# Kernel optimization log

Measured on AMD Instinct MI355X. Metric: run time of the kernel, lower is better.

The kernel has to match this reference:

```python
import jax, jax.numpy as jnp
import numpy as np

B, S = 2, 1024          # 2 sequences of 1024 tokens (prefill)
HID = 2880
HQ, HKV, D = 64, 8, 64  # query heads, kv heads, head_dim
W = 128                 # sliding window size
THETA = 150000.0
SCALE = D ** -0.5
Q_SIZE, KV_SIZE = HQ * D, HKV * D


def _rope_neox(pos, x):
    # pos: [T] int, x: [T, H, D] -> neox-style full-dim rotary
    half = D // 2
    inv_freq = 1.0 / (THETA ** (jnp.arange(half, dtype=jnp.float32) * 2.0 / D))
    ang = pos.astype(jnp.float32)[:, None] * inv_freq          # [T, D/2]
    cos = jnp.cos(ang)[:, None, :]                             # [T, 1, D/2]
    sin = jnp.sin(ang)[:, None, :]
    x1, x2 = x[..., :half], x[..., half:]
    return jnp.concatenate([x1 * cos - x2 * sin, x1 * sin + x2 * cos], axis=-1)


def setup_inputs() -> dict:
    key = jax.random.key(0)
    ks = jax.random.split(key, 10)
    s = 0.02
    hidden_states = jax.random.normal(ks[0], (B * S, HID), dtype=jnp.float32)
    positions = jnp.tile(jnp.arange(S, dtype=jnp.int32), B)    # per-sequence positions
    Wq = jax.random.normal(ks[1], (HID, Q_SIZE), dtype=jnp.float32) * s
    bq = jax.random.normal(ks[2], (Q_SIZE,), dtype=jnp.float32) * s
    Wk = jax.random.normal(ks[3], (HID, KV_SIZE), dtype=jnp.float32) * s
    bk = jax.random.normal(ks[4], (KV_SIZE,), dtype=jnp.float32) * s
    Wv = jax.random.normal(ks[5], (HID, KV_SIZE), dtype=jnp.float32) * s
    bv = jax.random.normal(ks[6], (KV_SIZE,), dtype=jnp.float32) * s
    Wo = jax.random.normal(ks[7], (Q_SIZE, HID), dtype=jnp.float32) * s
    bo = jax.random.normal(ks[8], (HID,), dtype=jnp.float32) * s
    return {"hidden_states": hidden_states, "positions": positions,
            "Wq": Wq, "bq": bq, "Wk": Wk, "bk": bk,
            "Wv": Wv, "bv": bv, "Wo": Wo, "bo": bo}


def reference(hidden_states, positions, Wq, bq, Wk, bk, Wv, bv, Wo, bo):
    T = hidden_states.shape[0]
    q = (hidden_states @ Wq + bq).reshape(T, HQ, D)
    k = (hidden_states @ Wk + bk).reshape(T, HKV, D)
    v = (hidden_states @ Wv + bv).reshape(T, HKV, D)
    q = _rope_neox(positions, q)
    k = _rope_neox(positions, k)

    # sliding-window causal attention (banded, window = last W keys + self)
    G = HQ // HKV  # GQA group size
    q5 = q.reshape(B, S, HKV, G, D)
    k4 = k.reshape(B, S, HKV, D)
    v4 = v.reshape(B, S, HKV, D)
    offs = jnp.arange(W + 1)
    idx = jnp.arange(S)[:, None] - W + offs[None, :]           # [S, W+1] key index j
    valid = idx >= 0                                           # causal+window band
    idx_c = jnp.clip(idx, 0, S - 1)
    kw = k4[:, idx_c]                                          # [B, S, W+1, HKV, D]
    vw = v4[:, idx_c]
    scores = jnp.einsum('bikgd,biwkd->bikgw', q5, kw) * SCALE  # [B,S,HKV,G,W+1]
    scores = jnp.where(valid[None, :, None, None, :], scores, jnp.float32(-1e30))
    p = jax.nn.softmax(scores, axis=-1)
    o = jnp.einsum('bikgw,biwkd->bikgd', p, vw).reshape(T, Q_SIZE)
    return o @ Wo + bo


if __name__ == '__main__':
    out = reference(**setup_inputs())
    print(out.shape, out.dtype)
```

## Files before the change

### kernel.cpp

```cpp
#include <hip/hip_runtime.h>

#define T_TOK 2048
#define S_LEN 1024
#define HIDN  2880
#define NHQ   64
#define NHKV  8
#define DH    64
#define QSZ   4096
#define KVSZ  512
#define WIN   128
#define NQKV  5120
#define NOPAD 2944

typedef __attribute__((ext_vector_type(4))) float f32x4;
typedef __attribute__((ext_vector_type(8))) short bf16x8;
typedef __attribute__((ext_vector_type(4))) short s16x4;

__device__ __forceinline__ unsigned short f2bf(float f) {
  unsigned u = __float_as_uint(f);
  u += 0x7fffu + ((u >> 16) & 1u);
  return (unsigned short)(u >> 16);
}
__device__ __forceinline__ float bf2f(unsigned short s) {
  return __uint_as_float(((unsigned)s) << 16);
}
__device__ __forceinline__ void ld_g2l16(const void* g, void* l) {
  __builtin_amdgcn_global_load_lds(
      (const __attribute__((address_space(1))) unsigned int*)g,
      (__attribute__((address_space(3))) unsigned int*)l, 16, 0, 0);
}

__global__ __launch_bounds__(256) void convert_hidden(
    const float* __restrict__ in, unsigned short* __restrict__ out)
{
  const size_t off = ((size_t)blockIdx.x * 256 + threadIdx.x) * 8;
  const f32x4 a = *(const f32x4*)(in + off);
  const f32x4 b = *(const f32x4*)(in + off + 4);
  bf16x8 p;
  p[0] = (short)f2bf(a[0]); p[1] = (short)f2bf(a[1]);
  p[2] = (short)f2bf(a[2]); p[3] = (short)f2bf(a[3]);
  p[4] = (short)f2bf(b[0]); p[5] = (short)f2bf(b[1]);
  p[6] = (short)f2bf(b[2]); p[7] = (short)f2bf(b[3]);
  *(bf16x8*)(out + off) = p;
}

__global__ __launch_bounds__(256) void transpose_w(
    const float* __restrict__ W, unsigned short* __restrict__ WT,
    int K, int N)
{
  __shared__ float tile[32][65];
  const int tid = threadIdx.x;
  const int nb = blockIdx.x * 64;
  const int kb = blockIdx.y * 32;
  {
    const int n2 = (tid & 31) * 2;
    const int k0 = tid >> 5;
    #pragma unroll
    for (int r = 0; r < 4; ++r) {
      const int k = k0 + r * 8;
      const int gn = nb + n2;
      const size_t base = (size_t)(kb + k) * N;
      tile[k][n2]     = (gn     < N) ? W[base + gn]     : 0.f;
      tile[k][n2 + 1] = (gn + 1 < N) ? W[base + gn + 1] : 0.f;
    }
  }
  __syncthreads();
  {
    const int k4 = (tid & 7) * 4;
    const int n0 = tid >> 3;
    #pragma unroll
    for (int r = 0; r < 2; ++r) {
      const int n = n0 + r * 32;
      s16x4 p;
      p[0] = (short)f2bf(tile[k4][n]);     p[1] = (short)f2bf(tile[k4 + 1][n]);
      p[2] = (short)f2bf(tile[k4 + 2][n]); p[3] = (short)f2bf(tile[k4 + 3][n]);
      *(s16x4*)(WT + (size_t)(nb + n) * K + kb + k4) = p;
    }
  }
}

__device__ __forceinline__ void gemm_core(
    const unsigned short* __restrict__ A, const unsigned short* __restrict__ BT,
    int K, int m0, int n0, unsigned short* As, unsigned short* Bs,
    f32x4 acc[4][4])
{
  const int tid  = threadIdx.x;
  const int lane = tid & 63;
  const int wid  = tid >> 6;
  const int wm = (wid >> 1) * 64;
  const int wn = (wid & 1) * 64;
  const int fr = lane & 15;
  const int fq = lane >> 4;

  const int rsub = tid >> 3;
  const int cg   = (tid & 7) ^ (rsub & 7);
  const unsigned short* Ap = A  + (size_t)(m0 + rsub) * K + cg * 8;
  const unsigned short* Bp = BT + (size_t)(n0 + rsub) * K + cg * 8;
  const size_t rstep = (size_t)32 * K;

  for (int k0 = 0; k0 < K; k0 += 64) {
    #pragma unroll
    for (int i = 0; i < 4; ++i) {
      ld_g2l16(Ap + i * rstep + k0, As + ((size_t)i * 256 + tid) * 8);
      ld_g2l16(Bp + i * rstep + k0, Bs + ((size_t)i * 256 + tid) * 8);
    }
    __syncthreads();
    #pragma unroll
    for (int ks = 0; ks < 2; ++ks) {
      const int kc = ks * 4 + fq;
      bf16x8 af[4], bfr[4];
      #pragma unroll
      for (int mt = 0; mt < 4; ++mt) {
        const int R = wm + mt * 16 + fr;
        af[mt] = *(const bf16x8*)(As + R * 64 + ((kc ^ (R & 7)) << 3));
      }
      #pragma unroll
      for (int nt = 0; nt < 4; ++nt) {
        const int R = wn + nt * 16 + fr;
        bfr[nt] = *(const bf16x8*)(Bs + R * 64 + ((kc ^ (R & 7)) << 3));
      }
      #pragma unroll
      for (int mt = 0; mt < 4; ++mt)
        #pragma unroll
        for (int nt = 0; nt < 4; ++nt)
          acc[mt][nt] = __builtin_amdgcn_mfma_f32_16x16x32_bf16(
              af[mt], bfr[nt], acc[mt][nt], 0, 0, 0);
    }
    __syncthreads();
  }
}

__device__ __forceinline__ void rope_epilogue(
    f32x4 acc[4][4], const float* __restrict__ bias,
    const int* __restrict__ pos, unsigned short* __restrict__ outp,
    int outStride, int colbase, int rowbase, int lane)
{
  const int fr = lane & 15;
  const int r4 = (lane >> 4) * 4;
  const float invf0 = exp2f((float)fr        * (-17.19460283f / 32.0f));
  const float invf1 = exp2f((float)(fr + 16) * (-17.19460283f / 32.0f));
  #pragma unroll
  for (int mt = 0; mt < 4; ++mt) {
    #pragma unroll
    for (int i = 0; i < 4; ++i) {
      const int m = rowbase + mt * 16 + r4 + i;
      const float p = (float)pos[m];
      #pragma unroll
      for (int ntp = 0; ntp < 2; ++ntp) {
        float sv, cv;
        __sincosf(p * (ntp ? invf1 : invf0), &sv, &cv);
        const int c1 = colbase + ntp * 16 + fr;
        const float x1 = acc[mt][ntp][i]     + bias[c1];
        const float x2 = acc[mt][ntp + 2][i] + bias[c1 + 32];
        outp[(size_t)m * outStride + c1]      = f2bf(x1 * cv - x2 * sv);
        outp[(size_t)m * outStride + c1 + 32] = f2bf(x1 * sv + x2 * cv);
      }
    }
  }
}

__global__ __launch_bounds__(256) void gemm_qkv(
    const unsigned short* __restrict__ A, const unsigned short* __restrict__ BT,
    const float* __restrict__ bq, const float* __restrict__ bk,
    const float* __restrict__ bv, const int* __restrict__ pos,
    unsigned short* __restrict__ qb, unsigned short* __restrict__ kb,
    unsigned short* __restrict__ vT)
{
  __shared__ unsigned short As[128 * 64];
  __shared__ unsigned short Bs[128 * 64];
  const int m0 = blockIdx.y * 128;
  const int n0 = blockIdx.x * 128;
  f32x4 acc[4][4];
  #pragma unroll
  for (int i = 0; i < 4; ++i)
    #pragma unroll
    for (int j = 0; j < 4; ++j) acc[i][j] = (f32x4){0.f, 0.f, 0.f, 0.f};
  gemm_core(A, BT, HIDN, m0, n0, As, Bs, acc);

  const int lane = threadIdx.x & 63;
  const int wid  = threadIdx.x >> 6;
  const int wm = (wid >> 1) * 64;
  const int wn = (wid & 1) * 64;
  const int fr = lane & 15;
  const int r4 = (lane >> 4) * 4;

  if (n0 < QSZ) {
    rope_epilogue(acc, bq, pos, qb, QSZ, n0 + wn, m0 + wm, lane);
  } else if (n0 < QSZ + KVSZ) {
    rope_epilogue(acc, bk, pos, kb, KVSZ, n0 - QSZ + wn, m0 + wm, lane);
  } else {
    #pragma unroll
    for (int nt = 0; nt < 4; ++nt) {
      const int vrow = n0 - (QSZ + KVSZ) + wn + nt * 16 + fr;
      const float bvv = bv[vrow];
      #pragma unroll
      for (int mt = 0; mt < 4; ++mt) {
        const int mb = m0 + wm + mt * 16 + r4;
        s16x4 p;
        p[0] = (short)f2bf(acc[mt][nt][0] + bvv);
        p[1] = (short)f2bf(acc[mt][nt][1] + bvv);
        p[2] = (short)f2bf(acc[mt][nt][2] + bvv);
        p[3] = (short)f2bf(acc[mt][nt][3] + bvv);
        *(s16x4*)(vT + (size_t)vrow * T_TOK + mb) = p;
      }
    }
  }
}

__global__ __launch_bounds__(256) void gemm_o(
    const unsigned short* __restrict__ A, const unsigned short* __restrict__ BT,
    const float* __restrict__ bias, float* __restrict__ C)
{
  __shared__ unsigned short As[128 * 64];
  __shared__ unsigned short Bs[128 * 64];
  const int m0 = blockIdx.y * 128;
  const int n0 = blockIdx.x * 128;
  f32x4 acc[4][4];
  #pragma unroll
  for (int i = 0; i < 4; ++i)
    #pragma unroll
    for (int j = 0; j < 4; ++j) acc[i][j] = (f32x4){0.f, 0.f, 0.f, 0.f};
  gemm_core(A, BT, QSZ, m0, n0, As, Bs, acc);

  const int lane = threadIdx.x & 63;
  const int wid  = threadIdx.x >> 6;
  const int wm = (wid >> 1) * 64;
  const int wn = (wid & 1) * 64;
  const int fr = lane & 15;
  const int r4 = (lane >> 4) * 4;
  #pragma unroll
  for (int nt = 0; nt < 4; ++nt) {
    const int n = n0 + wn + nt * 16 + fr;
    if (n >= HIDN) continue;
    const float bvv = bias[n];
    #pragma unroll
    for (int mt = 0; mt < 4; ++mt) {
      const int mb = m0 + wm + mt * 16 + r4;
      #pragma unroll
      for (int i = 0; i < 4; ++i)
        C[(size_t)(mb + i) * HIDN + n] = acc[mt][nt][i] + bvv;
    }
  }
}

__global__ __launch_bounds__(256) void attn_kernel(
    const unsigned short* __restrict__ q, const unsigned short* __restrict__ k,
    const unsigned short* __restrict__ vT, unsigned short* __restrict__ o)
{
  __shared__ unsigned short lds[26624];
  unsigned short* Ks = lds;
  unsigned short* Qs = lds + 13824;
  unsigned short* Ps = lds + 13824;
  unsigned short* Vt = lds;

  const int tid  = threadIdx.x;
  const int lane = tid & 63;
  const int wid  = tid >> 6;
  const int sq0  = blockIdx.x * 64;
  const int h    = blockIdx.y;
  const int b    = blockIdx.z;
  const int kvh  = h >> 3;
  const int kp0  = sq0 - WIN;

  #pragma unroll
  for (int j = 0; j < 2; ++j) {
    const int c  = tid + j * 256;
    const int qr = c >> 3, dc = (c & 7) * 8;
    const bf16x8 vv = *(const bf16x8*)(
        q + (size_t)(b * S_LEN + sq0 + qr) * QSZ + h * DH + dc);
    *(bf16x8*)&Qs[qr * 72 + dc] = vv;
  }
  #pragma unroll
  for (int j = 0; j < 6; ++j) {
    const int c  = tid + j * 256;
    const int kr = c >> 3, dc = (c & 7) * 8;
    int tok = b * S_LEN + kp0 + kr;
    if (tok < 0) tok = 0;
    const bf16x8 vv = *(const bf16x8*)(k + (size_t)tok * KVSZ + kvh * DH + dc);
    *(bf16x8*)&Ks[kr * 72 + dc] = vv;
  }
  __syncthreads();

  const int fr = lane & 15;
  const int fk = (lane >> 4) * 8;
  const int qw = wid * 16;

  f32x4 S[12];
  #pragma unroll
  for (int i = 0; i < 12; ++i) S[i] = (f32x4){0.f, 0.f, 0.f, 0.f};
  #pragma unroll
  for (int ks = 0; ks < 2; ++ks) {
    const bf16x8 af = *(const bf16x8*)&Qs[(qw + fr) * 72 + ks * 32 + fk];
    #pragma unroll
    for (int nt = 0; nt < 12; ++nt) {
      const bf16x8 bfr = *(const bf16x8*)&Ks[(nt * 16 + fr) * 72 + ks * 32 + fk];
      S[nt] = __builtin_amdgcn_mfma_f32_16x16x32_bf16(af, bfr, S[nt], 0, 0, 0);
    }
  }

  const int qbase = sq0 + qw + ((lane >> 4) << 2);
  float lsum[4] = {0.f, 0.f, 0.f, 0.f};
  #pragma unroll
  for (int nt = 0; nt < 12; ++nt) {
    const int jpos = kp0 + nt * 16 + fr;
    #pragma unroll
    for (int i = 0; i < 4; ++i) {
      const int qa = qbase + i;
      const bool valid = (jpos >= 0) && (jpos <= qa) && (jpos >= qa - WIN);
      const float e = valid ? __expf(S[nt][i] * 0.125f) : 0.f;
      S[nt][i] = e;
      lsum[i] += e;
    }
  }
  #pragma unroll
  for (int off = 1; off < 16; off <<= 1)
    #pragma unroll
    for (int i = 0; i < 4; ++i)
      lsum[i] += __shfl_xor(lsum[i], off, 64);
  float inv[4];
  #pragma unroll
  for (int i = 0; i < 4; ++i) inv[i] = 1.0f / lsum[i];

  __syncthreads();

  #pragma unroll
  for (int nt = 0; nt < 12; ++nt)
    #pragma unroll
    for (int i = 0; i < 4; ++i)
      Ps[(qbase - sq0 + i) * 200 + nt * 16 + fr] = f2bf(S[nt][i]);

  if (kp0 >= 0) {
    #pragma unroll
    for (int j = 0; j < 6; ++j) {
      const int c  = tid + j * 256;
      const int dr = c / 24, kc = (c % 24) * 8;
      const bf16x8 vv = *(const bf16x8*)(
          vT + (size_t)(kvh * DH + dr) * T_TOK + b * S_LEN + kp0 + kc);
      *(bf16x8*)&Vt[dr * 200 + kc] = vv;
    }
  } else {
    #pragma unroll
    for (int j = 0; j < 6; ++j) {
      const int c  = tid + j * 256;
      const int dr = c / 24, kc = (c % 24) * 8;
      bf16x8 vv;
      #pragma unroll
      for (int u = 0; u < 8; ++u) {
        int col = b * S_LEN + kp0 + kc + u;
        if (col < 0) col = 0;
        vv[u] = (short)vT[(size_t)(kvh * DH + dr) * T_TOK + col];
      }
      *(bf16x8*)&Vt[dr * 200 + kc] = vv;
    }
  }
  __syncthreads();

  f32x4 O[4];
  #pragma unroll
  for (int i = 0; i < 4; ++i) O[i] = (f32x4){0.f, 0.f, 0.f, 0.f};
  #pragma unroll
  for (int ks = 0; ks < 6; ++ks) {
    const bf16x8 pa = *(const bf16x8*)&Ps[(qw + fr) * 200 + ks * 32 + fk];
    #pragma unroll
    for (int nt = 0; nt < 4; ++nt) {
      const bf16x8 vb = *(const bf16x8*)&Vt[(nt * 16 + fr) * 200 + ks * 32 + fk];
      O[nt] = __builtin_amdgcn_mfma_f32_16x16x32_bf16(pa, vb, O[nt], 0, 0, 0);
    }
  }
  #pragma unroll
  for (int nt = 0; nt < 4; ++nt)
    #pragma unroll
    for (int i = 0; i < 4; ++i)
      o[(size_t)(b * S_LEN + qbase + i) * QSZ + h * DH + nt * 16 + fr] =
          f2bf(O[nt][i] * inv[i]);
}

extern "C" void kernel_launch(void* const* d_in, const int* in_sizes, int n_in,
                              void* d_out, int out_size, void* d_ws, size_t ws_size,
                              hipStream_t stream) {
  const float* hidden    = (const float*)d_in[0];
  const int*   positions = (const int*)d_in[1];
  const float* Wq = (const float*)d_in[2];
  const float* bq = (const float*)d_in[3];
  const float* Wk = (const float*)d_in[4];
  const float* bk = (const float*)d_in[5];
  const float* Wv = (const float*)d_in[6];
  const float* bv = (const float*)d_in[7];
  const float* Wo = (const float*)d_in[8];
  const float* bo = (const float*)d_in[9];
  float* out = (float*)d_out;

  char* ws = (char*)d_ws;
  unsigned short* hbf   = (unsigned short*)(ws);
  unsigned short* WqkvT = (unsigned short*)(ws + 11796480);
  unsigned short* qb    = (unsigned short*)(ws + 41287680);
  unsigned short* kb    = (unsigned short*)(ws + 58064896);
  unsigned short* vTb   = (unsigned short*)(ws + 60162048);

  const dim3 blk(256);
  convert_hidden<<<dim3((T_TOK * HIDN) / 2048), blk, 0, stream>>>(hidden, hbf);
  transpose_w<<<dim3(QSZ / 64, HIDN / 32), blk, 0, stream>>>(
      Wq, WqkvT, HIDN, QSZ);
  transpose_w<<<dim3(KVSZ / 64, HIDN / 32), blk, 0, stream>>>(
      Wk, WqkvT + (size_t)QSZ * HIDN, HIDN, KVSZ);
  transpose_w<<<dim3(KVSZ / 64, HIDN / 32), blk, 0, stream>>>(
      Wv, WqkvT + (size_t)(QSZ + KVSZ) * HIDN, HIDN, KVSZ);

  gemm_qkv<<<dim3(NQKV / 128, T_TOK / 128), blk, 0, stream>>>(
      hbf, WqkvT, bq, bk, bv, positions, qb, kb, vTb);

  transpose_w<<<dim3(NOPAD / 64, QSZ / 32), blk, 0, stream>>>(
      Wo, WqkvT, QSZ, HIDN);

  attn_kernel<<<dim3(S_LEN / 64, NHQ, 2), blk, 0, stream>>>(qb, kb, vTb, qb);
  gemm_o<<<dim3(NOPAD / 128, T_TOK / 128), blk, 0, stream>>>(
      qb, WqkvT, bo, out);
}
```

Baseline: 400.2 us.

## Vectorize weight transpose, process two heads per attention block, shrink gemm_o tiles

transpose_w now reads eight floats per thread with vector loads, with a scalar fallback for the partial edge tile, and writes bf16x8 stores. The attention kernel processes two query heads per block so each K/V window load serves both heads, and Q fragments are loaded straight into registers instead of through LDS. gemm_o switches to 64x128 tiles with 128 threads, doubling the grid to improve CU occupancy for the small output GEMM. In exchange attention holds twice the score registers, and gemm_o loads each B tile for fewer output rows.

```diff
diff --git a/kernel.cpp b/kernel.cpp
--- a/kernel.cpp
+++ b/kernel.cpp
@@ -48,35 +48,29 @@
     const float* __restrict__ W, unsigned short* __restrict__ WT,
     int K, int N)
 {
-  __shared__ float tile[32][65];
+  __shared__ float tile[32][72];
   const int tid = threadIdx.x;
   const int nb = blockIdx.x * 64;
   const int kb = blockIdx.y * 32;
-  {
-    const int n2 = (tid & 31) * 2;
-    const int k0 = tid >> 5;
-    #pragma unroll
-    for (int r = 0; r < 4; ++r) {
-      const int k = k0 + r * 8;
-      const int gn = nb + n2;
-      const size_t base = (size_t)(kb + k) * N;
-      tile[k][n2]     = (gn     < N) ? W[base + gn]     : 0.f;
-      tile[k][n2 + 1] = (gn + 1 < N) ? W[base + gn + 1] : 0.f;
-    }
-  }
-  __syncthreads();
-  {
-    const int k4 = (tid & 7) * 4;
-    const int n0 = tid >> 3;
-    #pragma unroll
-    for (int r = 0; r < 2; ++r) {
-      const int n = n0 + r * 32;
-      s16x4 p;
-      p[0] = (short)f2bf(tile[k4][n]);     p[1] = (short)f2bf(tile[k4 + 1][n]);
-      p[2] = (short)f2bf(tile[k4 + 2][n]); p[3] = (short)f2bf(tile[k4 + 3][n]);
-      *(s16x4*)(WT + (size_t)(nb + n) * K + kb + k4) = p;
-    }
-  }
+  const int kk = tid >> 3;
+  const int n8 = (tid & 7) * 8;
+  if (nb + 64 <= N) {
+    const float* src = W + (size_t)(kb + kk) * N + nb + n8;
+    *(f32x4*)&tile[kk][n8]     = *(const f32x4*)(src);
+    *(f32x4*)&tile[kk][n8 + 4] = *(const f32x4*)(src + 4);
+  } else {
+    #pragma unroll
+    for (int u = 0; u < 8; ++u)
+      tile[kk][n8 + u] = (nb + n8 + u < N)
+          ? W[(size_t)(kb + kk) * N + nb + n8 + u] : 0.f;
+  }
+  __syncthreads();
+  const int n  = tid & 63;
+  const int k8 = (tid >> 6) * 8;
+  bf16x8 p;
+  #pragma unroll
+  for (int j = 0; j < 8; ++j) p[j] = (short)f2bf(tile[k8 + j][n]);
+  *(bf16x8*)(WT + (size_t)(nb + n) * K + kb + k8) = p;
 }
 
 __device__ __forceinline__ void gemm_core(
@@ -207,26 +201,65 @@
   }
 }
 
-__global__ __launch_bounds__(256) void gemm_o(
+__global__ __launch_bounds__(128) void gemm_o(
     const unsigned short* __restrict__ A, const unsigned short* __restrict__ BT,
     const float* __restrict__ bias, float* __restrict__ C)
 {
-  __shared__ unsigned short As[128 * 64];
+  __shared__ unsigned short As[64 * 64];
   __shared__ unsigned short Bs[128 * 64];
-  const int m0 = blockIdx.y * 128;
+  const int tid  = threadIdx.x;
+  const int lane = tid & 63;
+  const int wid  = tid >> 6;
+  const int m0 = blockIdx.y * 64;
   const int n0 = blockIdx.x * 128;
+  const int wn = wid * 64;
+  const int fr = lane & 15;
+  const int fq = lane >> 4;
+
   f32x4 acc[4][4];
   #pragma unroll
   for (int i = 0; i < 4; ++i)
     #pragma unroll
     for (int j = 0; j < 4; ++j) acc[i][j] = (f32x4){0.f, 0.f, 0.f, 0.f};
-  gemm_core(A, BT, QSZ, m0, n0, As, Bs, acc);
-
-  const int lane = threadIdx.x & 63;
-  const int wid  = threadIdx.x >> 6;
-  const int wm = (wid >> 1) * 64;
-  const int wn = (wid & 1) * 64;
-  const int fr = lane & 15;
+
+  const int rsub = tid >> 3;
+  const int cg   = (tid & 7) ^ (rsub & 7);
+  const unsigned short* Ap = A  + (size_t)(m0 + rsub) * QSZ + cg * 8;
+  const unsigned short* Bp = BT + (size_t)(n0 + rsub) * QSZ + cg * 8;
+  const size_t rstep = (size_t)16 * QSZ;
+
+  for (int k0 = 0; k0 < QSZ; k0 += 64) {
+    #pragma unroll
+    for (int i = 0; i < 4; ++i)
+      ld_g2l16(Ap + i * rstep + k0, As + ((size_t)i * 128 + tid) * 8);
+    #pragma unroll
+    for (int i = 0; i < 8; ++i)
+      ld_g2l16(Bp + i * rstep + k0, Bs + ((size_t)i * 128 + tid) * 8);
+    __syncthreads();
+    #pragma unroll
+    for (int ks = 0; ks < 2; ++ks) {
+      const int kc = ks * 4 + fq;
+      bf16x8 af[4], bfr[4];
+      #pragma unroll
+      for (int mt = 0; mt < 4; ++mt) {
+        const int R = mt * 16 + fr;
+        af[mt] = *(const bf16x8*)(As + R * 64 + ((kc ^ (R & 7)) << 3));
+      }
+      #pragma unroll
+      for (int nt = 0; nt < 4; ++nt) {
+        const int R = wn + nt * 16 + fr;
+        bfr[nt] = *(const bf16x8*)(Bs + R * 64 + ((kc ^ (R & 7)) << 3));
+      }
+      #pragma unroll
+      for (int mt = 0; mt < 4; ++mt)
+        #pragma unroll
+        for (int nt = 0; nt < 4; ++nt)
+          acc[mt][nt] = __builtin_amdgcn_mfma_f32_16x16x32_bf16(
+              af[mt], bfr[nt], acc[mt][nt], 0, 0, 0);
+    }
+    __syncthreads();
+  }
+
   const int r4 = (lane >> 4) * 4;
   #pragma unroll
   for (int nt = 0; nt < 4; ++nt) {
@@ -235,7 +268,7 @@
     const float bvv = bias[n];
     #pragma unroll
     for (int mt = 0; mt < 4; ++mt) {
-      const int mb = m0 + wm + mt * 16 + r4;
+      const int mb = m0 + mt * 16 + r4;
       #pragma unroll
       for (int i = 0; i < 4; ++i)
         C[(size_t)(mb + i) * HIDN + n] = acc[mt][nt][i] + bvv;
@@ -243,33 +276,39 @@
   }
 }
 
-__global__ __launch_bounds__(256) void attn_kernel(
+__global__ __launch_bounds__(256, 3) void attn_kernel(
     const unsigned short* __restrict__ q, const unsigned short* __restrict__ k,
     const unsigned short* __restrict__ vT, unsigned short* __restrict__ o)
 {
   __shared__ unsigned short lds[26624];
   unsigned short* Ks = lds;
-  unsigned short* Qs = lds + 13824;
+  unsigned short* Vt = lds;
   unsigned short* Ps = lds + 13824;
-  unsigned short* Vt = lds;
 
   const int tid  = threadIdx.x;
   const int lane = tid & 63;
   const int wid  = tid >> 6;
   const int sq0  = blockIdx.x * 64;
-  const int h    = blockIdx.y;
+  const int hp   = blockIdx.y;
   const int b    = blockIdx.z;
-  const int kvh  = h >> 3;
+  const int h0   = hp * 2;
+  const int kvh  = hp >> 2;
   const int kp0  = sq0 - WIN;
 
-  #pragma unroll
-  for (int j = 0; j < 2; ++j) {
-    const int c  = tid + j * 256;
-    const int qr = c >> 3, dc = (c & 7) * 8;
-    const bf16x8 vv = *(const bf16x8*)(
-        q + (size_t)(b * S_LEN + sq0 + qr) * QSZ + h * DH + dc);
-    *(bf16x8*)&Qs[qr * 72 + dc] = vv;
-  }
+  const int fr = lane & 15;
+  const int fk = (lane >> 4) * 8;
+  const int qw = wid * 16;
+
+  bf16x8 qf[2][2];
+  {
+    const size_t qrow = (size_t)(b * S_LEN + sq0 + qw + fr) * QSZ;
+    #pragma unroll
+    for (int hh = 0; hh < 2; ++hh)
+      #pragma unroll
+      for (int ks2 = 0; ks2 < 2; ++ks2)
+        qf[hh][ks2] = *(const bf16x8*)(q + qrow + (h0 + hh) * DH + ks2 * 32 + fk);
+  }
+
   #pragma unroll
   for (int j = 0; j < 6; ++j) {
     const int c  = tid + j * 256;
@@ -281,25 +320,25 @@
   }
   __syncthreads();
 
-  const int fr = lane & 15;
-  const int fk = (lane >> 4) * 8;
-  const int qw = wid * 16;
-
-  f32x4 S[12];
-  #pragma unroll
-  for (int i = 0; i < 12; ++i) S[i] = (f32x4){0.f, 0.f, 0.f, 0.f};
-  #pragma unroll
-  for (int ks = 0; ks < 2; ++ks) {
-    const bf16x8 af = *(const bf16x8*)&Qs[(qw + fr) * 72 + ks * 32 + fk];
+  f32x4 S0[12], S1[12];
+  #pragma unroll
+  for (int i = 0; i < 12; ++i) {
+    S0[i] = (f32x4){0.f, 0.f, 0.f, 0.f};
+    S1[i] = (f32x4){0.f, 0.f, 0.f, 0.f};
+  }
+  #pragma unroll
+  for (int ks2 = 0; ks2 < 2; ++ks2) {
     #pragma unroll
     for (int nt = 0; nt < 12; ++nt) {
-      const bf16x8 bfr = *(const bf16x8*)&Ks[(nt * 16 + fr) * 72 + ks * 32 + fk];
-      S[nt] = __builtin_amdgcn_mfma_f32_16x16x32_bf16(af, bfr, S[nt], 0, 0, 0);
+      const bf16x8 bfr = *(const bf16x8*)&Ks[(nt * 16 + fr) * 72 + ks2 * 32 + fk];
+      S0[nt] = __builtin_amdgcn_mfma_f32_16x16x32_bf16(qf[0][ks2], bfr, S0[nt], 0, 0, 0);
+      S1[nt] = __builtin_amdgcn_mfma_f32_16x16x32_bf16(qf[1][ks2], bfr, S1[nt], 0, 0, 0);
     }
   }
 
   const int qbase = sq0 + qw + ((lane >> 4) << 2);
-  float lsum[4] = {0.f, 0.f, 0.f, 0.f};
+  float ls0[4] = {0.f, 0.f, 0.f, 0.f};
+  float ls1[4] = {0.f, 0.f, 0.f, 0.f};
   #pragma unroll
   for (int nt = 0; nt < 12; ++nt) {
     const int jpos = kp0 + nt * 16 + fr;
@@ -307,28 +346,32 @@
     for (int i = 0; i < 4; ++i) {
       const int qa = qbase + i;
       const bool valid = (jpos >= 0) && (jpos <= qa) && (jpos >= qa - WIN);
-      const float e = valid ? __expf(S[nt][i] * 0.125f) : 0.f;
-      S[nt][i] = e;
-      lsum[i] += e;
+      const float e0 = valid ? __expf(S0[nt][i] * 0.125f) : 0.f;
+      const float e1 = valid ? __expf(S1[nt][i] * 0.125f) : 0.f;
+      S0[nt][i] = e0; ls0[i] += e0;
+      S1[nt][i] = e1; ls1[i] += e1;
     }
   }
   #pragma unroll
   for (int off = 1; off < 16; off <<= 1)
     #pragma unroll
+    for (int i = 0; i < 4; ++i) {
+      ls0[i] += __shfl_xor(ls0[i], off, 64);
+      ls1[i] += __shfl_xor(ls1[i], off, 64);
+    }
+  float inv0[4], inv1[4];
+  #pragma unroll
+  for (int i = 0; i < 4; ++i) {
+    inv0[i] = 1.0f / ls0[i];
+    inv1[i] = 1.0f / ls1[i];
+  }
+  __syncthreads();
+
+  #pragma unroll
+  for (int nt = 0; nt < 12; ++nt)
+    #pragma unroll
     for (int i = 0; i < 4; ++i)
-      lsum[i] += __shfl_xor(lsum[i], off, 64);
-  float inv[4];
-  #pragma unroll
-  for (int i = 0; i < 4; ++i) inv[i] = 1.0f / lsum[i];
-
-  __syncthreads();
-
-  #pragma unroll
-  for (int nt = 0; nt < 12; ++nt)
-    #pragma unroll
-    for (int i = 0; i < 4; ++i)
-      Ps[(qbase - sq0 + i) * 200 + nt * 16 + fr] = f2bf(S[nt][i]);
-
+      Ps[(qbase - sq0 + i) * 200 + nt * 16 + fr] = f2bf(S0[nt][i]);
   if (kp0 >= 0) {
     #pragma unroll
     for (int j = 0; j < 6; ++j) {
@@ -355,24 +398,55 @@
   }
   __syncthreads();
 
-  f32x4 O[4];
-  #pragma unroll
-  for (int i = 0; i < 4; ++i) O[i] = (f32x4){0.f, 0.f, 0.f, 0.f};
-  #pragma unroll
-  for (int ks = 0; ks < 6; ++ks) {
-    const bf16x8 pa = *(const bf16x8*)&Ps[(qw + fr) * 200 + ks * 32 + fk];
-    #pragma unroll
-    for (int nt = 0; nt < 4; ++nt) {
-      const bf16x8 vb = *(const bf16x8*)&Vt[(nt * 16 + fr) * 200 + ks * 32 + fk];
-      O[nt] = __builtin_amdgcn_mfma_f32_16x16x32_bf16(pa, vb, O[nt], 0, 0, 0);
-    }
-  }
-  #pragma unroll
-  for (int nt = 0; nt < 4; ++nt)
+  {
+    f32x4 O[4];
+    #pragma unroll
+    for (int i = 0; i < 4; ++i) O[i] = (f32x4){0.f, 0.f, 0.f, 0.f};
+    #pragma unroll
+    for (int ks2 = 0; ks2 < 6; ++ks2) {
+      const bf16x8 pa = *(const bf16x8*)&Ps[(qw + fr) * 200 + ks2 * 32 + fk];
+      #pragma unroll
+      for (int nt = 0; nt < 4; ++nt) {
+        const bf16x8 vb = *(const bf16x8*)&Vt[(nt * 16 + fr) * 200 + ks2 * 32 + fk];
+        O[nt] = __builtin_amdgcn_mfma_f32_16x16x32_bf16(pa, vb, O[nt], 0, 0, 0);
+      }
+    }
+    #pragma unroll
+    for (int nt = 0; nt < 4; ++nt)
+      #pragma unroll
+      for (int i = 0; i < 4; ++i)
+        o[(size_t)(b * S_LEN + qbase + i) * QSZ + h0 * DH + nt * 16 + fr] =
+            f2bf(O[nt][i] * inv0[i]);
+  }
+  __syncthreads();
+
+  #pragma unroll
+  for (int nt = 0; nt < 12; ++nt)
     #pragma unroll
     for (int i = 0; i < 4; ++i)
-      o[(size_t)(b * S_LEN + qbase + i) * QSZ + h * DH + nt * 16 + fr] =
-          f2bf(O[nt][i] * inv[i]);
+      Ps[(qbase - sq0 + i) * 200 + nt * 16 + fr] = f2bf(S1[nt][i]);
+  __syncthreads();
+
+  {
+    f32x4 O[4];
+    #pragma unroll
+    for (int i = 0; i < 4; ++i) O[i] = (f32x4){0.f, 0.f, 0.f, 0.f};
+    #pragma unroll
+    for (int ks2 = 0; ks2 < 6; ++ks2) {
+      const bf16x8 pa = *(const bf16x8*)&Ps[(qw + fr) * 200 + ks2 * 32 + fk];
+      #pragma unroll
+      for (int nt = 0; nt < 4; ++nt) {
+        const bf16x8 vb = *(const bf16x8*)&Vt[(nt * 16 + fr) * 200 + ks2 * 32 + fk];
+        O[nt] = __builtin_amdgcn_mfma_f32_16x16x32_bf16(pa, vb, O[nt], 0, 0, 0);
+      }
+    }
+    #pragma unroll
+    for (int nt = 0; nt < 4; ++nt)
+      #pragma unroll
+      for (int i = 0; i < 4; ++i)
+        o[(size_t)(b * S_LEN + qbase + i) * QSZ + (h0 + 1) * DH + nt * 16 + fr] =
+            f2bf(O[nt][i] * inv1[i]);
+  }
 }
 
 extern "C" void kernel_launch(void* const* d_in, const int* in_sizes, int n_in,
@@ -412,7 +486,8 @@
   transpose_w<<<dim3(NOPAD / 64, QSZ / 32), blk, 0, stream>>>(
       Wo, WqkvT, QSZ, HIDN);
 
-  attn_kernel<<<dim3(S_LEN / 64, NHQ, 2), blk, 0, stream>>>(qb, kb, vTb, qb);
-  gemm_o<<<dim3(NOPAD / 128, T_TOK / 128), blk, 0, stream>>>(
+  attn_kernel<<<dim3(S_LEN / 64, NHQ / 2, 2), blk, 0, stream>>>(
+      qb, kb, vTb, qb);
+  gemm_o<<<dim3(NOPAD / 128, T_TOK / 64), dim3(128), 0, stream>>>(
       qb, WqkvT, bo, out);
 }
```

Measured after the change: 396.5 us. Within noise of the previous version (-0.9%).
